# Kernel tuning notes

Hardware: AMD Instinct MI355X
Metric: run time of the kernel (lower is better)

Reference implementation:

```python
import jax, jax.numpy as jnp
import numpy as np

N_NODES = 50000
N_EDGES = 800000
NUM_GRAPHS = 512
EMB = 128
OUT_DIM = 2145 * 2
EPS_BN = 1e-5
EPS_GN = 1e-5


def gat_conv(x, src, dst, W, att_s, att_d, bias, n):
    # PyG GATConv, heads=1: h = x W ; alpha_e = leakyrelu(a_s.h[src] + a_d.h[dst])
    h = x @ W                                   # [N, EMB]
    a_s = h @ att_s                             # [N]
    a_d = h @ att_d                             # [N]
    logits = jax.nn.leaky_relu(a_s[src] + a_d[dst], 0.2)   # [E]
    m = jax.ops.segment_max(logits, dst, num_segments=n)
    ex = jnp.exp(logits - m[dst])
    denom = jax.ops.segment_sum(ex, dst, num_segments=n)
    alpha = ex / (denom[dst] + 1e-16)           # segment softmax over in-edges
    out = jax.ops.segment_sum(alpha[:, None] * h[src], dst, num_segments=n)
    return out + bias


def setup_inputs() -> dict:
    key = jax.random.key(0)
    ks = jax.random.split(key, 16)
    x = jax.random.normal(ks[0], (N_NODES, 1), dtype=jnp.float32)
    edge_index = jax.random.randint(ks[1], (2, N_EDGES), 0, N_NODES, dtype=jnp.int64)
    batch = jnp.sort(jax.random.randint(ks[2], (N_NODES,), 0, NUM_GRAPHS, dtype=jnp.int64))
    edge_attr = jax.random.normal(ks[3], (N_EDGES, 1), dtype=jnp.float32)
    s = 0.1
    return {
        "x": x, "edge_index": edge_index, "batch": batch, "edge_attr": edge_attr,
        "W0": jax.random.normal(ks[4], (1, EMB), dtype=jnp.float32) * s,
        "as0": jax.random.normal(ks[5], (EMB,), dtype=jnp.float32) * s,
        "ad0": jax.random.normal(ks[6], (EMB,), dtype=jnp.float32) * s,
        "b0": jnp.zeros((EMB,), dtype=jnp.float32),
        "W1": jax.random.normal(ks[7], (EMB, EMB), dtype=jnp.float32) * s,
        "as1": jax.random.normal(ks[8], (EMB,), dtype=jnp.float32) * s,
        "ad1": jax.random.normal(ks[9], (EMB,), dtype=jnp.float32) * s,
        "b1": jnp.zeros((EMB,), dtype=jnp.float32),
        "bn_g": jnp.ones((EMB,), dtype=jnp.float32),
        "bn_b": jnp.zeros((EMB,), dtype=jnp.float32),
        "gn_w": jnp.ones((EMB,), dtype=jnp.float32),
        "gn_b": jnp.zeros((EMB,), dtype=jnp.float32),
        "gn_ms": jnp.ones((EMB,), dtype=jnp.float32),
        "Wout": jax.random.normal(ks[10], (2 * EMB, OUT_DIM), dtype=jnp.float32) * s,
        "bout": jnp.zeros((OUT_DIM,), dtype=jnp.float32),
    }


def reference(x, edge_index, batch, edge_attr, W0, as0, ad0, b0, W1, as1, ad1, b1,
              bn_g, bn_b, gn_w, gn_b, gn_ms, Wout, bout):
    n = x.shape[0]
    # PyG GATConv add_self_loops=True
    loops = jnp.arange(n, dtype=edge_index.dtype)
    src = jnp.concatenate([edge_index[0], loops])
    dst = jnp.concatenate([edge_index[1], loops])
    # edge_attr ignored (edge_dim=None in GATConv)

    h = jnp.tanh(gat_conv(x, src, dst, W0, as0, ad0, b0, n))
    # dropout p=0.2 treated as identity (deterministic eval reference)

    # BatchNorm over nodes (training/batch statistics)
    mu = jnp.mean(h, axis=0)
    var = jnp.mean((h - mu) ** 2, axis=0)
    h = bn_g * (h - mu) / jnp.sqrt(var + EPS_BN) + bn_b

    # GraphNorm: per-graph mean-scale normalization
    cnt = jax.ops.segment_sum(jnp.ones((n,), h.dtype), batch, num_segments=NUM_GRAPHS)[:, None]
    gmean = jax.ops.segment_sum(h, batch, num_segments=NUM_GRAPHS) / cnt
    h0 = h - gmean[batch] * gn_ms
    gvar = jax.ops.segment_sum(h0 ** 2, batch, num_segments=NUM_GRAPHS) / cnt
    h = gn_w * h0 / jnp.sqrt(gvar[batch] + EPS_GN) + gn_b

    h = jnp.tanh(gat_conv(h, src, dst, W1, as1, ad1, b1, n))

    # global max + mean pool per graph
    pmax = jax.ops.segment_max(h, batch, num_segments=NUM_GRAPHS)
    pmean = jax.ops.segment_sum(h, batch, num_segments=NUM_GRAPHS) / cnt
    pooled = jnp.concatenate([pmax, pmean], axis=1)   # [G, 2*EMB]
    return pooled @ Wout + bout                        # [G, OUT_DIM]
```

## Files before the change

kernel.cpp:

```cpp
#include <hip/hip_runtime.h>
#include <hip/hip_fp16.h>
#include <math.h>

#define EMB 128
#define NGRAPH 512
#define MAXBUCK 800
#define BCAP 1536
#define CHUNK 8192

typedef _Float16 f16_t;
typedef _Float16 f16x8 __attribute__((ext_vector_type(8)));
typedef float f32x4 __attribute__((ext_vector_type(4)));

__device__ __forceinline__ float leaky(float v){ return v > 0.f ? v : 0.2f*v; }
__device__ __forceinline__ float ftanh(float x){
    float u = __expf(2.f*x);
    return 1.f - 2.f*__builtin_amdgcn_rcpf(u + 1.f);
}
__device__ __forceinline__ float frcp(float x){ return __builtin_amdgcn_rcpf(x); }

__global__ void k_prep(const float* W0, const float* as0, const float* ad0, float* c_sd){
    __shared__ float s1[128], s2[128];
    int t = threadIdx.x;
    float w = W0[t];
    s1[t] = w * as0[t]; s2[t] = w * ad0[t];
    __syncthreads();
    for(int off=64; off>0; off>>=1){
        if(t<off){ s1[t]+=s1[t+off]; s2[t]+=s2[t+off]; }
        __syncthreads();
    }
    if(t==0){ c_sd[0]=s1[0]; c_sd[1]=s2[0]; }
}

__global__ void k_w1h(const float* W1, f16_t* W1t){
    int idx = blockIdx.x*blockDim.x+threadIdx.x;
    int n = idx>>7, k = idx&127;
    W1t[n*128+k] = (f16_t)W1[k*128+n];
}

__global__ void k_wouth(const float* Wout, int OUT, f16_t* WoutT){
    __shared__ f16_t lt[64*68];
    int t = threadIdx.x;
    int n0 = blockIdx.x*64, k0 = blockIdx.y*64;
    #pragma unroll
    for(int j=0;j<16;j++){
        int k_l = (t>>6)*16 + j;
        int n_l = t&63;
        int n = n0+n_l;
        float v = (n < OUT) ? Wout[(size_t)(k0+k_l)*OUT + n] : 0.f;
        lt[n_l*68 + k_l] = (f16_t)v;
    }
    __syncthreads();
    #pragma unroll
    for(int j=0;j<16;j++){
        int n_l = (t>>6)*16 + j;
        int k_l = t&63;
        WoutT[(size_t)(n0+n_l)*256 + k0 + k_l] = lt[n_l*68 + k_l];
    }
}

__global__ void k_bcount(const int* dst, int E, int nbuck, int* bcnt){
    __shared__ int h[MAXBUCK];
    int t = threadIdx.x;
    for(int j=t;j<MAXBUCK;j+=512) h[j]=0;
    __syncthreads();
    int stride = gridDim.x*blockDim.x;
    for(int e = blockIdx.x*blockDim.x+t; e<E; e+=stride)
        atomicAdd(&h[dst[e]>>6], 1);
    __syncthreads();
    for(int j=t;j<nbuck;j+=512) if(h[j]) atomicAdd(&bcnt[j], h[j]);
}

__global__ void k_bscan(const int* bcnt, int nbuck, int* bbase, int* bcursor){
    __shared__ int s[1024];
    int t = threadIdx.x;
    int own = (t<nbuck)? bcnt[t] : 0;
    s[t] = own;
    __syncthreads();
    for(int off=1; off<1024; off<<=1){
        int a = (t>=off)? s[t-off] : 0;
        __syncthreads();
        s[t] += a;
        __syncthreads();
    }
    if(t<nbuck){ int ex = s[t]-own; bbase[t]=ex; bcursor[t]=ex; }
    if(t==nbuck-1) bbase[nbuck]=s[t];
}

__global__ __launch_bounds__(512) void k_bscatter(const int* src, const int* dst, int E,
                                                  int nbuck, int* bcursor, unsigned* ebuf){
    __shared__ int cnt[MAXBUCK];
    __shared__ int loff[MAXBUCK];
    __shared__ int cur[MAXBUCK];
    __shared__ int gbase[MAXBUCK];
    __shared__ int s[1024];
    __shared__ unsigned srt[CHUNK];
    int t = threadIdx.x;
    int c0 = blockIdx.x*CHUNK;
    int m = E - c0; if(m > CHUNK) m = CHUNK;
    for(int j=t;j<MAXBUCK;j+=512) cnt[j]=0;
    __syncthreads();
    unsigned rec[16];
    #pragma unroll
    for(int u=0;u<16;u++){
        int j = u*512 + t;
        if(j<m){
            int d = dst[c0+j];
            int sv = src[c0+j];
            rec[u] = ((unsigned)(d>>6)<<22) | ((unsigned)(d&63)<<16) | (unsigned)sv;
            atomicAdd(&cnt[d>>6], 1);
        } else rec[u] = 0xFFFFFFFFu;
    }
    __syncthreads();
    int v0 = (t<nbuck)? cnt[t]:0;
    int j2 = t+512;
    int v1 = (j2<nbuck)? cnt[j2]:0;
    s[t]=v0; s[j2]=v1;
    __syncthreads();
    for(int off=1; off<1024; off<<=1){
        int a = (t>=off)? s[t-off]:0;
        int b = s[j2-off];
        __syncthreads();
        s[t]+=a; s[j2]+=b;
        __syncthreads();
    }
    for(int j=t;j<nbuck;j+=512){
        int c = cnt[j];
        int ex = s[j]-c;
        loff[j]=ex; cur[j]=ex;
        if(c>0) gbase[j]=atomicAdd(&bcursor[j], c);
    }
    __syncthreads();
    #pragma unroll
    for(int u=0;u<16;u++){
        if(rec[u]!=0xFFFFFFFFu){
            int b = rec[u]>>22;
            int p = atomicAdd(&cur[b],1);
            srt[p]=rec[u];
        }
    }
    __syncthreads();
    for(int j=t;j<m;j+=512){
        unsigned r = srt[j];
        int b = r>>22;
        ebuf[gbase[b] + (j - loff[b])] = r;
    }
}

__global__ void k_gseg(const int* batch, int N, int* gstart){
    int i = blockIdx.x*blockDim.x+threadIdx.x;
    if(i>=N) return;
    int b = batch[i];
    if(i==0){ for(int g=0;g<=b;g++) gstart[g]=0; }
    else { int bp=batch[i-1]; for(int g=bp+1; g<=b; g++) gstart[g]=i; }
    if(i==N-1){ for(int g=b+1; g<=NGRAPH; g++) gstart[g]=N; }
}

__global__ __launch_bounds__(256) void k_gat0(const unsigned* ebuf, const int* bbase,
                                              const float* x, const float* c_sd,
                                              int N, float* s0,
                                              unsigned short* csr16, int* rowstart){
    __shared__ unsigned raw[BCAP];
    __shared__ unsigned short esrc[BCAP];
    __shared__ int cnt[64], off[64], cur[64];
    int t = threadIdx.x;
    int b = blockIdx.x;
    int e0 = bbase[b];
    int m = bbase[b+1]-e0; if(m>BCAP) m=BCAP;
    for(int j=t;j<m;j+=256) raw[j]=ebuf[e0+j];
    if(t<64) cnt[t]=0;
    __syncthreads();
    for(int j=t;j<m;j+=256) atomicAdd(&cnt[(raw[j]>>16)&63],1);
    __syncthreads();
    if(t<64){
        int v = cnt[t]; int inc = v;
        #pragma unroll
        for(int o=1;o<64;o<<=1){ int u = __shfl_up(inc,o); if(t>=o) inc+=u; }
        off[t]=inc-v; cur[t]=inc-v;
    }
    __syncthreads();
    for(int j=t;j<m;j+=256){
        unsigned r=raw[j]; int n=(r>>16)&63;
        int p=atomicAdd(&cur[n],1);
        esrc[p]=(unsigned short)(r&0xFFFF);
    }
    __syncthreads();
    for(int j=t;j<m;j+=256) csr16[e0+j]=esrc[j];
    if(t<64) rowstart[b*64+t] = e0 + off[t];
    int n = t>>2, sub = t&3;
    int gid = b*64 + n;
    if(gid>=N) return;
    float cs=c_sd[0], cd=c_sd[1];
    float xi = x[gid]; float adi = cd*xi;
    int r0=off[n], r1=cur[n];
    float den=0.f, num=0.f;
    if(sub==0){
        float ex = __expf(leaky(fmaf(cs,xi,adi)));
        den=ex; num=ex*xi;
    }
    for(int e=r0+sub;e<r1;e+=4){
        float xs = x[esrc[e]];
        float ee = __expf(leaky(fmaf(cs,xs,adi)));
        den += ee; num = fmaf(ee,xs,num);
    }
    den += __shfl_xor(den,1); den += __shfl_xor(den,2);
    num += __shfl_xor(num,1); num += __shfl_xor(num,2);
    if(sub==0) s0[gid] = num*frcp(den+1e-16f);
}

__global__ void k_gstats(const float* s0, const int* gstart, const float* W0, const float* b0,
                         float* gsum, float* gsumsq){
    int g=blockIdx.x, k=threadIdx.x;
    float wk=W0[k], bk=b0[k];
    int i0=gstart[g], i1=gstart[g+1];
    float s=0.f, q=0.f;
    for(int i=i0;i<i1;i++){
        float t=ftanh(fmaf(s0[i],wk,bk));
        s+=t; q=fmaf(t,t,q);
    }
    gsum[g*EMB+k]=s; gsumsq[g*EMB+k]=q;
}

__global__ void k_bnstats(const float* gsum, const float* gsumsq,
                          const float* bn_g, const float* bn_b, int N,
                          float* bnsc, float* bnsh){
    int k=threadIdx.x;
    float cs=0.f, cq=0.f;
    for(int g=0; g<NGRAPH; g++){ cs+=gsum[g*EMB+k]; cq+=gsumsq[g*EMB+k]; }
    float invN = 1.f/(float)N;
    float mu=cs*invN; float var = cq*invN - mu*mu;
    float sc = bn_g[k]*rsqrtf(var+1e-5f);
    bnsc[k]=sc; bnsh[k]=bn_b[k]-mu*sc;
}

__global__ void k_pq(const float* gsum, const float* gsumsq, const int* gstart,
                     const float* bnsc, const float* bnsh,
                     const float* gn_w, const float* gn_b, const float* gn_ms,
                     float* P, float* Q){
    int idx = blockIdx.x*blockDim.x+threadIdx.x;
    int g = idx>>7, k = idx&127;
    int c = gstart[g+1]-gstart[g];
    float rc = frcp((float)(c>0?c:1));
    float m1 = gsum[idx]*rc, m2 = gsumsq[idx]*rc;
    float A = bnsc[k], Bs = bnsh[k];
    float gmean = fmaf(A,m1,Bs);
    float B = Bs - gmean*gn_ms[k];
    float gvar = A*A*m2 + 2.f*A*B*m1 + B*B;
    float rg = rsqrtf(gvar+1e-5f);
    float w = gn_w[k];
    P[idx] = w*A*rg;
    Q[idx] = fmaf(w*B, rg, gn_b[k]);
}

__global__ void k_H(const float* s0, const int* batch, const float* W0, const float* b0,
                    const float* P, const float* Q, int N, f16_t* H){
    int total = N*16;
    int stride = gridDim.x*blockDim.x;
    for(int idx = blockIdx.x*blockDim.x+threadIdx.x; idx < total; idx += stride){
        int i = idx>>4;
        int k0 = (idx&15)*8;
        float s = s0[i]; int g = batch[i];
        const float* Pg=&P[g*EMB+k0]; const float* Qg=&Q[g*EMB+k0];
        const float* W0p=&W0[k0]; const float* b0p=&b0[k0];
        f16x8 o;
        #pragma unroll
        for(int u=0;u<8;u++){
            o[u] = (f16_t)fmaf(Pg[u], ftanh(fmaf(s,W0p[u],b0p[u])), Qg[u]);
        }
        *(f16x8*)&H[(size_t)i*EMB + k0] = o;
    }
}

__global__ __launch_bounds__(256) void k_gemm1(const f16_t* H, const f16_t* W1t,
        const float* as1, const float* ad1,
        int N, f16_t* h1, float* a_s, float* a_d){
    __shared__ f16_t ob[64*136];
    int t = threadIdx.x;
    int i0 = blockIdx.x*64;
    int w = t>>6, l = t&63;
    int lm = l&15, lq = l>>4;
    int arow = i0 + w*16 + lm; if(arow > N-1) arow = N-1;
    const f16_t* ap = &H[(size_t)arow*EMB + lq*8];
    f16x8 a[4];
    #pragma unroll
    for(int kt=0;kt<4;kt++) a[kt] = *(const f16x8*)&ap[kt*32];
    f32x4 acc[8];
    #pragma unroll
    for(int nt=0;nt<8;nt++) acc[nt] = (f32x4){0.f,0.f,0.f,0.f};
    #pragma unroll
    for(int nt=0;nt<8;nt++){
        const f16_t* bp = &W1t[(nt*16 + lm)*128 + lq*8];
        f16x8 b0v = *(const f16x8*)&bp[0];
        f16x8 b1v = *(const f16x8*)&bp[32];
        f16x8 b2v = *(const f16x8*)&bp[64];
        f16x8 b3v = *(const f16x8*)&bp[96];
        acc[nt] = __builtin_amdgcn_mfma_f32_16x16x32_f16(a[0], b0v, acc[nt], 0, 0, 0);
        acc[nt] = __builtin_amdgcn_mfma_f32_16x16x32_f16(a[1], b1v, acc[nt], 0, 0, 0);
        acc[nt] = __builtin_amdgcn_mfma_f32_16x16x32_f16(a[2], b2v, acc[nt], 0, 0, 0);
        acc[nt] = __builtin_amdgcn_mfma_f32_16x16x32_f16(a[3], b3v, acc[nt], 0, 0, 0);
    }
    float ps[4] = {0.f,0.f,0.f,0.f};
    float pd[4] = {0.f,0.f,0.f,0.f};
    #pragma unroll
    for(int nt=0;nt<8;nt++){
        int n = nt*16 + lm;
        float asv = as1[n], adv = ad1[n];
        #pragma unroll
        for(int r=0;r<4;r++){
            ps[r] = fmaf(acc[nt][r], asv, ps[r]);
            pd[r] = fmaf(acc[nt][r], adv, pd[r]);
        }
    }
    #pragma unroll
    for(int r=0;r<4;r++){
        #pragma unroll
        for(int off=1; off<16; off<<=1){
            ps[r] += __shfl_xor(ps[r], off);
            pd[r] += __shfl_xor(pd[r], off);
        }
    }
    if(lm==0){
        #pragma unroll
        for(int r=0;r<4;r++){
            int i = i0 + w*16 + lq*4 + r;
            if(i < N){ a_s[i]=ps[r]; a_d[i]=pd[r]; }
        }
    }
    #pragma unroll
    for(int nt=0;nt<8;nt++){
        int n = nt*16 + lm;
        #pragma unroll
        for(int r=0;r<4;r++){
            int row = w*16 + lq*4 + r;
            ob[row*136 + n] = (f16_t)acc[nt][r];
        }
    }
    __syncthreads();
    #pragma unroll
    for(int c=0;c<4;c++){
        int idx = t + 256*c;
        int row = idx>>4, q = idx&15;
        int i = i0 + row;
        if(i < N){
            f16x8 v = *(const f16x8*)&ob[row*136 + q*8];
            *(f16x8*)&h1[(size_t)i*EMB + q*8] = v;
        }
    }
}

__global__ __launch_bounds__(256) void k_gat1(const unsigned short* csr16, const int* rowstart,
                                              const f16_t* h1, const float* a_s, const float* a_d,
                                              const float* b1, int N, f16_t* h2){
    int wave = threadIdx.x>>6, lane = threadIdx.x&63;
    int i = blockIdx.x*4 + wave;
    if(i>=N) return;
    int r0=rowstart[i], r1=rowstart[i+1]; int deg=r1-r0;
    float adi = a_d[i];
    float exs = __expf(leaky(a_s[i] + adi) - 4.f);
    const __half2* h1v = (const __half2*)h1;
    float2 hv = __half22float2(h1v[(size_t)i*64 + lane]);
    float2 acc0; acc0.x = exs*hv.x; acc0.y = exs*hv.y;
    float2 acc1 = {0.f,0.f}, acc2 = {0.f,0.f}, acc3 = {0.f,0.f};
    float denp = (lane==0)? exs : 0.f;
    for(int c=0;c<deg;c+=64){
        int e = c+lane;
        int s = 0; float ex = 0.f;
        if(e<deg){ s = (int)csr16[r0+e]; ex = __expf(leaky(a_s[s]+adi)-4.f); }
        denp += ex;
        int cnt = min(64, deg-c);
        int jj=0;
        for(; jj+3<cnt; jj+=4){
            float a0=__shfl(ex,jj);   int s0i=__shfl(s,jj);
            float a1=__shfl(ex,jj+1); int s1i=__shfl(s,jj+1);
            float a2=__shfl(ex,jj+2); int s2i=__shfl(s,jj+2);
            float a3=__shfl(ex,jj+3); int s3i=__shfl(s,jj+3);
            float2 v0 = __half22float2(h1v[(size_t)s0i*64 + lane]);
            float2 v1 = __half22float2(h1v[(size_t)s1i*64 + lane]);
            float2 v2 = __half22float2(h1v[(size_t)s2i*64 + lane]);
            float2 v3 = __half22float2(h1v[(size_t)s3i*64 + lane]);
            acc0.x = fmaf(a0, v0.x, acc0.x); acc0.y = fmaf(a0, v0.y, acc0.y);
            acc1.x = fmaf(a1, v1.x, acc1.x); acc1.y = fmaf(a1, v1.y, acc1.y);
            acc2.x = fmaf(a2, v2.x, acc2.x); acc2.y = fmaf(a2, v2.y, acc2.y);
            acc3.x = fmaf(a3, v3.x, acc3.x); acc3.y = fmaf(a3, v3.y, acc3.y);
        }
        for(; jj<cnt; jj++){
            float a0=__shfl(ex,jj); int s0i=__shfl(s,jj);
            float2 v0 = __half22float2(h1v[(size_t)s0i*64 + lane]);
            acc0.x = fmaf(a0, v0.x, acc0.x); acc0.y = fmaf(a0, v0.y, acc0.y);
        }
    }
    acc0.x += acc1.x + acc2.x + acc3.x;
    acc0.y += acc1.y + acc2.y + acc3.y;
    for(int o=32; o; o>>=1) denp += __shfl_xor(denp, o);
    float rden = frcp(denp + 1e-16f);
    float2 bb = *(const float2*)&b1[lane*2];
    float ox = ftanh(fmaf(acc0.x, rden, bb.x));
    float oy = ftanh(fmaf(acc0.y, rden, bb.y));
    *(__half2*)&h2[(size_t)i*EMB + lane*2] = __floats2half2_rn(ox, oy);
}

__global__ void k_pool(const f16_t* h2, const int* gstart, f16_t* pooled){
    int g=blockIdx.x, k=threadIdx.x;
    const __half2* h2v = (const __half2*)h2;
    int i0=gstart[g], i1=gstart[g+1];
    float2 mx = {-1e30f,-1e30f}, sm = {0.f,0.f};
    for(int i=i0;i<i1;i++){
        float2 v=__half22float2(h2v[(size_t)i*64+k]);
        mx.x=fmaxf(mx.x,v.x); mx.y=fmaxf(mx.y,v.y);
        sm.x+=v.x; sm.y+=v.y;
    }
    float c = frcp((float)((i1-i0)>0 ? (i1-i0) : 1));
    pooled[g*256+2*k  ]=(f16_t)mx.x;
    pooled[g*256+2*k+1]=(f16_t)mx.y;
    pooled[g*256+128+2*k  ]=(f16_t)(sm.x*c);
    pooled[g*256+128+2*k+1]=(f16_t)(sm.y*c);
}

__global__ __launch_bounds__(256) void k_out(const f16_t* pooled, const f16_t* WoutT,
                                             const float* bout, int OUT, float* out){
    int t = threadIdx.x;
    int w = t>>6, l = t&63;
    int lm = l&15, lq = l>>4;
    int m0 = (blockIdx.y*4 + w)*16;
    int n0 = blockIdx.x*64;
    f16x8 a[8];
    const f16_t* ap = &pooled[(m0+lm)*256 + lq*8];
    #pragma unroll
    for(int kt=0;kt<8;kt++) a[kt] = *(const f16x8*)&ap[kt*32];
    f32x4 acc[4];
    #pragma unroll
    for(int nt=0;nt<4;nt++) acc[nt] = (f32x4){0.f,0.f,0.f,0.f};
    #pragma unroll
    for(int nt=0;nt<4;nt++){
        const f16_t* bp = &WoutT[(size_t)(n0 + nt*16 + lm)*256 + lq*8];
        #pragma unroll
        for(int kt=0;kt<8;kt++){
            f16x8 b = *(const f16x8*)&bp[kt*32];
            acc[nt] = __builtin_amdgcn_mfma_f32_16x16x32_f16(a[kt], b, acc[nt], 0, 0, 0);
        }
    }
    #pragma unroll
    for(int nt=0;nt<4;nt++){
        int n = n0 + nt*16 + lm;
        if(n >= OUT) continue;
        float bv = bout[n];
        #pragma unroll
        for(int r=0;r<4;r++){
            int m = m0 + lq*4 + r;
            out[(size_t)m*OUT + n] = acc[nt][r] + bv;
        }
    }
}

extern "C" void kernel_launch(void* const* d_in, const int* in_sizes, int n_in,
                              void* d_out, int out_size, void* d_ws, size_t ws_size,
                              hipStream_t stream) {
    const float* x    = (const float*)d_in[0];
    const int*   eidx = (const int*)d_in[1];
    const int*   batch= (const int*)d_in[2];
    const float* W0   = (const float*)d_in[4];
    const float* as0  = (const float*)d_in[5];
    const float* ad0  = (const float*)d_in[6];
    const float* b0   = (const float*)d_in[7];
    const float* W1   = (const float*)d_in[8];
    const float* as1  = (const float*)d_in[9];
    const float* ad1  = (const float*)d_in[10];
    const float* b1   = (const float*)d_in[11];
    const float* bn_g = (const float*)d_in[12];
    const float* bn_b = (const float*)d_in[13];
    const float* gn_w = (const float*)d_in[14];
    const float* gn_b = (const float*)d_in[15];
    const float* gn_ms= (const float*)d_in[16];
    const float* Wout = (const float*)d_in[17];
    const float* bout = (const float*)d_in[18];

    int N = in_sizes[0];
    int E = in_sizes[1]/2;
    int OUT = out_size / NGRAPH;
    const int* srcp = eidx;
    const int* dstp = eidx + E;
    int nbuck = (N+63)>>6;

    char* w = (char*)d_ws;
    auto alloc = [&](size_t bytes) -> void* {
        void* p = (void*)w; w += (bytes+255)&~(size_t)255; return p;
    };
    int* bcnt     = (int*)alloc(MAXBUCK*4);
    int* bbase    = (int*)alloc((MAXBUCK+1)*4);
    int* bcursor  = (int*)alloc(MAXBUCK*4);
    unsigned* ebuf= (unsigned*)alloc((size_t)E*4);
    unsigned short* csr16 = (unsigned short*)alloc((size_t)E*2);
    int* rowstart = (int*)alloc((size_t)(MAXBUCK*64+64)*4);
    float* c_sd   = (float*)alloc(256);
    float* s0     = (float*)alloc((size_t)N*4);
    int* gstart   = (int*)alloc((NGRAPH+1)*4);
    float* gsum   = (float*)alloc(NGRAPH*EMB*4);
    float* gsq    = (float*)alloc(NGRAPH*EMB*4);
    float* bnsc   = (float*)alloc(512);
    float* bnsh   = (float*)alloc(512);
    float* P      = (float*)alloc(NGRAPH*EMB*4);
    float* Q      = (float*)alloc(NGRAPH*EMB*4);
    f16_t* Hbuf   = (f16_t*)alloc((size_t)N*EMB*2);
    f16_t* h1     = (f16_t*)alloc((size_t)N*EMB*2);
    f16_t* h2     = (f16_t*)alloc((size_t)N*EMB*2);
    float* a_sv   = (float*)alloc((size_t)N*4);
    float* a_dv   = (float*)alloc((size_t)N*4);
    f16_t* pooled = (f16_t*)alloc(NGRAPH*256*2);
    f16_t* w1t    = (f16_t*)alloc(128*128*2);
    f16_t* woutt  = (f16_t*)alloc((size_t)4352*256*2);

    hipMemsetAsync(bcnt, 0, MAXBUCK*4, stream);

    k_prep<<<1,128,0,stream>>>(W0,as0,ad0,c_sd);
    k_w1h<<<64,256,0,stream>>>(W1,w1t);
    dim3 wg(68,4);
    k_wouth<<<wg,256,0,stream>>>(Wout,OUT,woutt);
    k_bcount<<<120,512,0,stream>>>(dstp,E,nbuck,bcnt);
    k_bscan<<<1,1024,0,stream>>>(bcnt,nbuck,bbase,bcursor);
    int nchunk = (E+CHUNK-1)/CHUNK;
    k_bscatter<<<nchunk,512,0,stream>>>(srcp,dstp,E,nbuck,bcursor,ebuf);
    k_gseg<<<(N+255)/256,256,0,stream>>>(batch,N,gstart);
    k_gat0<<<nbuck,256,0,stream>>>(ebuf,bbase,x,c_sd,N,s0,csr16,rowstart);
    k_gstats<<<NGRAPH,128,0,stream>>>(s0,gstart,W0,b0,gsum,gsq);
    k_bnstats<<<1,128,0,stream>>>(gsum,gsq,bn_g,bn_b,N,bnsc,bnsh);
    k_pq<<<(NGRAPH*EMB)/256,256,0,stream>>>(gsum,gsq,gstart,bnsc,bnsh,gn_w,gn_b,gn_ms,P,Q);
    k_H<<<1024,256,0,stream>>>(s0,batch,W0,b0,P,Q,N,Hbuf);
    k_gemm1<<<(N+63)/64,256,0,stream>>>(Hbuf,w1t,as1,ad1,N,h1,a_sv,a_dv);
    k_gat1<<<(N+3)/4,256,0,stream>>>(csr16,rowstart,h1,a_sv,a_dv,b1,N,h2);
    k_pool<<<NGRAPH,64,0,stream>>>(h2,gstart,pooled);
    dim3 og(68, 8);
    k_out<<<og,256,0,stream>>>(pooled,woutt,bout,OUT,(float*)d_out);
}
```

Measured before the change: 194.8 us.

## Fuse prep kernels, merge gseg into scan, fuse H into GEMM, pack gather payload

Combines the three weight-prep kernels into one launch and folds the graph-segment computation into the single-block bucket scan. It also builds the normalized H tile straight into swizzled LDS inside the GEMM kernel, so the N×128 fp16 H buffer is no longer written and re-read. In the GAT aggregation, source index and fp16 attention weight are packed into one shuffle word and the loop is unrolled 8-way. Risks: gstart is now computed serially by one 1024-thread block, and the attention weights are rounded to fp16.

```diff
diff --git a/kernel.cpp b/kernel.cpp
--- a/kernel.cpp
+++ b/kernel.cpp
@@ -19,43 +19,42 @@
 }
 __device__ __forceinline__ float frcp(float x){ return __builtin_amdgcn_rcpf(x); }
 
-__global__ void k_prep(const float* W0, const float* as0, const float* ad0, float* c_sd){
+__global__ __launch_bounds__(256) void k_misc(const float* W0, const float* as0, const float* ad0,
+                                              float* c_sd, const float* W1, f16_t* W1t,
+                                              const float* Wout, int OUT, f16_t* WoutT){
+    __shared__ f16_t lt[64*68];
     __shared__ float s1[128], s2[128];
-    int t = threadIdx.x;
-    float w = W0[t];
-    s1[t] = w * as0[t]; s2[t] = w * ad0[t];
-    __syncthreads();
-    for(int off=64; off>0; off>>=1){
-        if(t<off){ s1[t]+=s1[t+off]; s2[t]+=s2[t+off]; }
+    int b = blockIdx.x;
+    int t = threadIdx.x;
+    if(b < 272){
+        int n0 = (b%68)*64, k0 = (b/68)*64;
+        #pragma unroll
+        for(int j=0;j<16;j++){
+            int k_l = (t>>6)*16 + j;
+            int n_l = t&63;
+            int n = n0+n_l;
+            float v = (n < OUT) ? Wout[(size_t)(k0+k_l)*OUT + n] : 0.f;
+            lt[n_l*68 + k_l] = (f16_t)v;
+        }
         __syncthreads();
-    }
-    if(t==0){ c_sd[0]=s1[0]; c_sd[1]=s2[0]; }
-}
-
-__global__ void k_w1h(const float* W1, f16_t* W1t){
-    int idx = blockIdx.x*blockDim.x+threadIdx.x;
-    int n = idx>>7, k = idx&127;
-    W1t[n*128+k] = (f16_t)W1[k*128+n];
-}
-
-__global__ void k_wouth(const float* Wout, int OUT, f16_t* WoutT){
-    __shared__ f16_t lt[64*68];
-    int t = threadIdx.x;
-    int n0 = blockIdx.x*64, k0 = blockIdx.y*64;
-    #pragma unroll
-    for(int j=0;j<16;j++){
-        int k_l = (t>>6)*16 + j;
-        int n_l = t&63;
-        int n = n0+n_l;
-        float v = (n < OUT) ? Wout[(size_t)(k0+k_l)*OUT + n] : 0.f;
-        lt[n_l*68 + k_l] = (f16_t)v;
-    }
-    __syncthreads();
-    #pragma unroll
-    for(int j=0;j<16;j++){
-        int n_l = (t>>6)*16 + j;
-        int k_l = t&63;
-        WoutT[(size_t)(n0+n_l)*256 + k0 + k_l] = lt[n_l*68 + k_l];
+        #pragma unroll
+        for(int j=0;j<16;j++){
+            int n_l = (t>>6)*16 + j;
+            int k_l = t&63;
+            WoutT[(size_t)(n0+n_l)*256 + k0 + k_l] = lt[n_l*68 + k_l];
+        }
+    } else if(b < 336){
+        int idx = (b-272)*256 + t;
+        int n = idx>>7, k = idx&127;
+        W1t[n*128+k] = (f16_t)W1[k*128+n];
+    } else {
+        if(t<128){ float w = W0[t]; s1[t]=w*as0[t]; s2[t]=w*ad0[t]; }
+        __syncthreads();
+        for(int off=64; off>0; off>>=1){
+            if(t<off){ s1[t]+=s1[t+off]; s2[t]+=s2[t+off]; }
+            __syncthreads();
+        }
+        if(t==0){ c_sd[0]=s1[0]; c_sd[1]=s2[0]; }
     }
 }
 
@@ -71,7 +70,8 @@
     for(int j=t;j<nbuck;j+=512) if(h[j]) atomicAdd(&bcnt[j], h[j]);
 }
 
-__global__ void k_bscan(const int* bcnt, int nbuck, int* bbase, int* bcursor){
+__global__ void k_bscan(const int* bcnt, int nbuck, int* bbase, int* bcursor,
+                        const int* batch, int N, int* gstart){
     __shared__ int s[1024];
     int t = threadIdx.x;
     int own = (t<nbuck)? bcnt[t] : 0;
@@ -85,6 +85,12 @@
     }
     if(t<nbuck){ int ex = s[t]-own; bbase[t]=ex; bcursor[t]=ex; }
     if(t==nbuck-1) bbase[nbuck]=s[t];
+    for(int i=t; i<N; i+=1024){
+        int b2 = batch[i];
+        if(i==0){ for(int g=0;g<=b2;g++) gstart[g]=0; }
+        else { int bp=batch[i-1]; for(int g=bp+1; g<=b2; g++) gstart[g]=i; }
+        if(i==N-1){ for(int g=b2+1; g<=NGRAPH; g++) gstart[g]=N; }
+    }
 }
 
 __global__ __launch_bounds__(512) void k_bscatter(const int* src, const int* dst, int E,
@@ -145,15 +151,6 @@
         int b = r>>22;
         ebuf[gbase[b] + (j - loff[b])] = r;
     }
-}
-
-__global__ void k_gseg(const int* batch, int N, int* gstart){
-    int i = blockIdx.x*blockDim.x+threadIdx.x;
-    if(i>=N) return;
-    int b = batch[i];
-    if(i==0){ for(int g=0;g<=b;g++) gstart[g]=0; }
-    else { int bp=batch[i-1]; for(int g=bp+1; g<=b; g++) gstart[g]=i; }
-    if(i==N-1){ for(int g=b+1; g<=NGRAPH; g++) gstart[g]=N; }
 }
 
 __global__ __launch_bounds__(256) void k_gat0(const unsigned* ebuf, const int* bbase,
@@ -252,38 +249,44 @@
     Q[idx] = fmaf(w*B, rg, gn_b[k]);
 }
 
-__global__ void k_H(const float* s0, const int* batch, const float* W0, const float* b0,
-                    const float* P, const float* Q, int N, f16_t* H){
-    int total = N*16;
-    int stride = gridDim.x*blockDim.x;
-    for(int idx = blockIdx.x*blockDim.x+threadIdx.x; idx < total; idx += stride){
-        int i = idx>>4;
-        int k0 = (idx&15)*8;
-        float s = s0[i]; int g = batch[i];
-        const float* Pg=&P[g*EMB+k0]; const float* Qg=&Q[g*EMB+k0];
-        const float* W0p=&W0[k0]; const float* b0p=&b0[k0];
-        f16x8 o;
-        #pragma unroll
-        for(int u=0;u<8;u++){
-            o[u] = (f16_t)fmaf(Pg[u], ftanh(fmaf(s,W0p[u],b0p[u])), Qg[u]);
-        }
-        *(f16x8*)&H[(size_t)i*EMB + k0] = o;
-    }
-}
-
-__global__ __launch_bounds__(256) void k_gemm1(const f16_t* H, const f16_t* W1t,
-        const float* as1, const float* ad1,
+__global__ __launch_bounds__(256) void k_gemm1(const float* s0, const int* batch,
+        const float* W0, const float* b0, const float* P, const float* Q,
+        const f16_t* W1t, const float* as1, const float* ad1,
         int N, f16_t* h1, float* a_s, float* a_d){
+    __shared__ f16_t A_lds[64*128];
     __shared__ f16_t ob[64*136];
     int t = threadIdx.x;
     int i0 = blockIdx.x*64;
+    #pragma unroll
+    for(int j=0;j<4;j++){
+        int c = t + 256*j;
+        int r = c>>4, q = c&15;
+        int i = i0 + r;
+        f16x8 chunk;
+        if(i < N){
+            float s = s0[i]; int g = batch[i];
+            int k0 = q*8;
+            const float* Pg=&P[g*EMB+k0]; const float* Qg=&Q[g*EMB+k0];
+            const float* W0p=&W0[k0]; const float* b0p=&b0[k0];
+            #pragma unroll
+            for(int u=0;u<8;u++)
+                chunk[u] = (f16_t)fmaf(Pg[u], ftanh(fmaf(s,W0p[u],b0p[u])), Qg[u]);
+        } else {
+            #pragma unroll
+            for(int u=0;u<8;u++) chunk[u] = (f16_t)0.f;
+        }
+        *(f16x8*)&A_lds[r*128 + ((q ^ (r&15))<<3)] = chunk;
+    }
+    __syncthreads();
     int w = t>>6, l = t&63;
     int lm = l&15, lq = l>>4;
-    int arow = i0 + w*16 + lm; if(arow > N-1) arow = N-1;
-    const f16_t* ap = &H[(size_t)arow*EMB + lq*8];
     f16x8 a[4];
     #pragma unroll
-    for(int kt=0;kt<4;kt++) a[kt] = *(const f16x8*)&ap[kt*32];
+    for(int kt=0;kt<4;kt++){
+        int r = w*16 + lm;
+        int q = kt*4 + lq;
+        a[kt] = *(const f16x8*)&A_lds[r*128 + ((q ^ (r&15))<<3)];
+    }
     f32x4 acc[8];
     #pragma unroll
     for(int nt=0;nt<8;nt++) acc[nt] = (f32x4){0.f,0.f,0.f,0.f};
@@ -364,28 +367,47 @@
     float denp = (lane==0)? exs : 0.f;
     for(int c=0;c<deg;c+=64){
         int e = c+lane;
-        int s = 0; float ex = 0.f;
-        if(e<deg){ s = (int)csr16[r0+e]; ex = __expf(leaky(a_s[s]+adi)-4.f); }
-        denp += ex;
+        unsigned pk = 0;
+        if(e<deg){
+            int s = (int)csr16[r0+e];
+            float ex = __expf(leaky(a_s[s]+adi)-4.f);
+            denp += ex;
+            pk = (unsigned)s | ((unsigned)__half_as_ushort(__float2half(ex))<<16);
+        }
         int cnt = min(64, deg-c);
         int jj=0;
-        for(; jj+3<cnt; jj+=4){
-            float a0=__shfl(ex,jj);   int s0i=__shfl(s,jj);
-            float a1=__shfl(ex,jj+1); int s1i=__shfl(s,jj+1);
-            float a2=__shfl(ex,jj+2); int s2i=__shfl(s,jj+2);
-            float a3=__shfl(ex,jj+3); int s3i=__shfl(s,jj+3);
-            float2 v0 = __half22float2(h1v[(size_t)s0i*64 + lane]);
-            float2 v1 = __half22float2(h1v[(size_t)s1i*64 + lane]);
-            float2 v2 = __half22float2(h1v[(size_t)s2i*64 + lane]);
-            float2 v3 = __half22float2(h1v[(size_t)s3i*64 + lane]);
+        for(; jj+7<cnt; jj+=8){
+            unsigned p0=__shfl(pk,jj+0), p1=__shfl(pk,jj+1), p2=__shfl(pk,jj+2), p3=__shfl(pk,jj+3);
+            unsigned p4=__shfl(pk,jj+4), p5=__shfl(pk,jj+5), p6=__shfl(pk,jj+6), p7=__shfl(pk,jj+7);
+            float2 v0 = __half22float2(h1v[(size_t)(p0&0xFFFF)*64 + lane]);
+            float2 v1 = __half22float2(h1v[(size_t)(p1&0xFFFF)*64 + lane]);
+            float2 v2 = __half22float2(h1v[(size_t)(p2&0xFFFF)*64 + lane]);
+            float2 v3 = __half22float2(h1v[(size_t)(p3&0xFFFF)*64 + lane]);
+            float2 v4 = __half22float2(h1v[(size_t)(p4&0xFFFF)*64 + lane]);
+            float2 v5 = __half22float2(h1v[(size_t)(p5&0xFFFF)*64 + lane]);
+            float2 v6 = __half22float2(h1v[(size_t)(p6&0xFFFF)*64 + lane]);
+            float2 v7 = __half22float2(h1v[(size_t)(p7&0xFFFF)*64 + lane]);
+            float a0=__half2float(__ushort_as_half((unsigned short)(p0>>16)));
+            float a1=__half2float(__ushort_as_half((unsigned short)(p1>>16)));
+            float a2=__half2float(__ushort_as_half((unsigned short)(p2>>16)));
+            float a3=__half2float(__ushort_as_half((unsigned short)(p3>>16)));
+            float a4=__half2float(__ushort_as_half((unsigned short)(p4>>16)));
+            float a5=__half2float(__ushort_as_half((unsigned short)(p5>>16)));
+            float a6=__half2float(__ushort_as_half((unsigned short)(p6>>16)));
+            float a7=__half2float(__ushort_as_half((unsigned short)(p7>>16)));
             acc0.x = fmaf(a0, v0.x, acc0.x); acc0.y = fmaf(a0, v0.y, acc0.y);
             acc1.x = fmaf(a1, v1.x, acc1.x); acc1.y = fmaf(a1, v1.y, acc1.y);
             acc2.x = fmaf(a2, v2.x, acc2.x); acc2.y = fmaf(a2, v2.y, acc2.y);
             acc3.x = fmaf(a3, v3.x, acc3.x); acc3.y = fmaf(a3, v3.y, acc3.y);
+            acc0.x = fmaf(a4, v4.x, acc0.x); acc0.y = fmaf(a4, v4.y, acc0.y);
+            acc1.x = fmaf(a5, v5.x, acc1.x); acc1.y = fmaf(a5, v5.y, acc1.y);
+            acc2.x = fmaf(a6, v6.x, acc2.x); acc2.y = fmaf(a6, v6.y, acc2.y);
+            acc3.x = fmaf(a7, v7.x, acc3.x); acc3.y = fmaf(a7, v7.y, acc3.y);
         }
         for(; jj<cnt; jj++){
-            float a0=__shfl(ex,jj); int s0i=__shfl(s,jj);
-            float2 v0 = __half22float2(h1v[(size_t)s0i*64 + lane]);
+            unsigned p0=__shfl(pk,jj);
+            float2 v0 = __half22float2(h1v[(size_t)(p0&0xFFFF)*64 + lane]);
+            float a0=__half2float(__ushort_as_half((unsigned short)(p0>>16)));
             acc0.x = fmaf(a0, v0.x, acc0.x); acc0.y = fmaf(a0, v0.y, acc0.y);
         }
     }
@@ -500,7 +522,6 @@
     float* bnsh   = (float*)alloc(512);
     float* P      = (float*)alloc(NGRAPH*EMB*4);
     float* Q      = (float*)alloc(NGRAPH*EMB*4);
-    f16_t* Hbuf   = (f16_t*)alloc((size_t)N*EMB*2);
     f16_t* h1     = (f16_t*)alloc((size_t)N*EMB*2);
     f16_t* h2     = (f16_t*)alloc((size_t)N*EMB*2);
     float* a_sv   = (float*)alloc((size_t)N*4);
@@ -511,21 +532,16 @@
 
     hipMemsetAsync(bcnt, 0, MAXBUCK*4, stream);
 
-    k_prep<<<1,128,0,stream>>>(W0,as0,ad0,c_sd);
-    k_w1h<<<64,256,0,stream>>>(W1,w1t);
-    dim3 wg(68,4);
-    k_wouth<<<wg,256,0,stream>>>(Wout,OUT,woutt);
+    k_misc<<<337,256,0,stream>>>(W0,as0,ad0,c_sd,W1,w1t,Wout,OUT,woutt);
     k_bcount<<<120,512,0,stream>>>(dstp,E,nbuck,bcnt);
-    k_bscan<<<1,1024,0,stream>>>(bcnt,nbuck,bbase,bcursor);
+    k_bscan<<<1,1024,0,stream>>>(bcnt,nbuck,bbase,bcursor,batch,N,gstart);
     int nchunk = (E+CHUNK-1)/CHUNK;
     k_bscatter<<<nchunk,512,0,stream>>>(srcp,dstp,E,nbuck,bcursor,ebuf);
-    k_gseg<<<(N+255)/256,256,0,stream>>>(batch,N,gstart);
     k_gat0<<<nbuck,256,0,stream>>>(ebuf,bbase,x,c_sd,N,s0,csr16,rowstart);
     k_gstats<<<NGRAPH,128,0,stream>>>(s0,gstart,W0,b0,gsum,gsq);
     k_bnstats<<<1,128,0,stream>>>(gsum,gsq,bn_g,bn_b,N,bnsc,bnsh);
     k_pq<<<(NGRAPH*EMB)/256,256,0,stream>>>(gsum,gsq,gstart,bnsc,bnsh,gn_w,gn_b,gn_ms,P,Q);
-    k_H<<<1024,256,0,stream>>>(s0,batch,W0,b0,P,Q,N,Hbuf);
-    k_gemm1<<<(N+63)/64,256,0,stream>>>(Hbuf,w1t,as1,ad1,N,h1,a_sv,a_dv);
+    k_gemm1<<<(N+63)/64,256,0,stream>>>(s0,batch,W0,b0,P,Q,w1t,as1,ad1,N,h1,a_sv,a_dv);
     k_gat1<<<(N+3)/4,256,0,stream>>>(csr16,rowstart,h1,a_sv,a_dv,b1,N,h2);
     k_pool<<<NGRAPH,64,0,stream>>>(h2,gstart,pooled);
     dim3 og(68, 8);
```

Measured after the change: 213.0 us. 1.09x slower.
